# Kernel optimization log

Measured on AMD Instinct MI355X. Metric: run time of the kernel, lower is better.

The kernel has to match this reference:

```python
import jax, jax.numpy as jnp
import numpy as np

N_NODES = 100000
N_EDGES = 1600000
NUM_RELS = 16
NUM_BASES = 8
IN_FEATS = 128
N_HIDDEN = 128
N_CLASSES = 40


def _make_layer_params(key, d_in, d_out):
    k0, k1, k2 = jax.random.split(key, 3)
    s_in = 1.0 / np.sqrt(d_in)
    bases = jax.random.normal(k0, (NUM_BASES, d_in, d_out), jnp.float32) * s_in
    comp = jax.random.normal(k1, (NUM_RELS, NUM_BASES), jnp.float32) * (1.0 / np.sqrt(NUM_BASES))
    root = jax.random.normal(k2, (d_in, d_out), jnp.float32) * s_in
    bias = jnp.zeros((d_out,), jnp.float32)
    return bases, comp, root, bias


def setup_inputs() -> dict:
    key = jax.random.key(0)
    ks = jax.random.split(key, 8)
    x = jax.random.normal(ks[0], (N_NODES, IN_FEATS), jnp.float32)
    edge_src = jax.random.randint(ks[1], (N_EDGES,), 0, N_NODES, dtype=jnp.int32)
    edge_dst = jax.random.randint(ks[2], (N_EDGES,), 0, N_NODES, dtype=jnp.int32)
    edge_type = jax.random.randint(ks[3], (N_EDGES,), 0, NUM_RELS, dtype=jnp.int32)
    bases0, comp0, root0, bias0 = _make_layer_params(ks[4], IN_FEATS, N_HIDDEN)
    bases1, comp1, root1, bias1 = _make_layer_params(ks[5], N_HIDDEN, N_HIDDEN)
    bases2, comp2, root2, bias2 = _make_layer_params(ks[6], N_HIDDEN, N_CLASSES)
    return dict(x=x, edge_src=edge_src, edge_dst=edge_dst, edge_type=edge_type,
                bases0=bases0, comp0=comp0, root0=root0, bias0=bias0,
                bases1=bases1, comp1=comp1, root1=root1, bias1=bias1,
                bases2=bases2, comp2=comp2, root2=root2, bias2=bias2)


def _rgcn_layer(x, edge_src, edge_dst, edge_type, bases, comp, root, bias):
    # basis decomposition: W_r = sum_b comp[r,b] * bases[b]   -> [R, d_in, d_out]
    W = jnp.einsum('rb,bio->rio', comp, bases)
    # transform all node features under every relation (R small, dense GEMMs)
    xw = jnp.einsum('ni,rio->rno', x, W)                    # [R, N, d_out]
    # per-edge message: gather by (relation, source) -- irregular access
    msg = xw[edge_type, edge_src]                           # [E, d_out]
    # mean aggregation per (destination, relation), as in PyG RGCNConv (aggr='mean')
    seg = edge_dst * NUM_RELS + edge_type                   # [E]
    deg = jax.ops.segment_sum(jnp.ones((msg.shape[0],), x.dtype), seg,
                              num_segments=N_NODES * NUM_RELS)
    norm = 1.0 / jnp.maximum(deg[seg], 1.0)                 # [E]
    agg = jax.ops.segment_sum(msg * norm[:, None], edge_dst, num_segments=N_NODES)
    return agg + x @ root + bias


def reference(x, edge_src, edge_dst, edge_type,
              bases0, comp0, root0, bias0,
              bases1, comp1, root1, bias1,
              bases2, comp2, root2, bias2):
    # dropout is identity at inference; activation='relu' on all but last layer
    h = _rgcn_layer(x, edge_src, edge_dst, edge_type, bases0, comp0, root0, bias0)
    h = jax.nn.relu(h)
    h = _rgcn_layer(h, edge_src, edge_dst, edge_type, bases1, comp1, root1, bias1)
    h = jax.nn.relu(h)
    h = _rgcn_layer(h, edge_src, edge_dst, edge_type, bases2, comp2, root2, bias2)
    return h
```

## Files before the change

kernel.cpp:

```cpp
#include <hip/hip_runtime.h>
#include <hip/hip_bf16.h>

#define NNODES 100000
#define NEDGES 1600000
#define NRELS 16
#define NBASES 8
#define DFEAT 128
#define NCLS 40
#define MAXDEG 64
#define KTOT 1152
#define KA   1024

typedef __attribute__((ext_vector_type(8))) short bf16x8v;
typedef __attribute__((ext_vector_type(4))) float f32x4v;
typedef __attribute__((ext_vector_type(2))) float f32x2v;
typedef __attribute__((ext_vector_type(4))) unsigned short u16x4;

struct __align__(8) bf16x4s { __hip_bfloat162 lo, hi; };

__global__ __launch_bounds__(256)
void k_pre(const float* __restrict__ x, __hip_bfloat16* __restrict__ xb,
           short* __restrict__ q8, float* __restrict__ qs,
           const int* __restrict__ esrc, const int* __restrict__ edst,
           const int* __restrict__ etyp,
           unsigned* __restrict__ degD, unsigned* __restrict__ ell)
{
    unsigned bid = blockIdx.x;
    if (bid % 17u == 0u) {
        int k = (int)(bid / 17u);
        int e0 = k * 1024 + ((int)threadIdx.x << 2);
        if (e0 < NEDGES) {
            int4 s4 = *(const int4*)(esrc + e0);
            int4 d4 = *(const int4*)(edst + e0);
            int4 t4 = *(const int4*)(etyp + e0);
            unsigned sl0 = atomicAdd(&degD[d4.x], 1u);
            unsigned sl1 = atomicAdd(&degD[d4.y], 1u);
            unsigned sl2 = atomicAdd(&degD[d4.z], 1u);
            unsigned sl3 = atomicAdd(&degD[d4.w], 1u);
            if (sl0 < MAXDEG) __builtin_nontemporal_store(
                ((unsigned)s4.x << 4) | (unsigned)t4.x, &ell[(size_t)d4.x * MAXDEG + sl0]);
            if (sl1 < MAXDEG) __builtin_nontemporal_store(
                ((unsigned)s4.y << 4) | (unsigned)t4.y, &ell[(size_t)d4.y * MAXDEG + sl1]);
            if (sl2 < MAXDEG) __builtin_nontemporal_store(
                ((unsigned)s4.z << 4) | (unsigned)t4.z, &ell[(size_t)d4.z * MAXDEG + sl2]);
            if (sl3 < MAXDEG) __builtin_nontemporal_store(
                ((unsigned)s4.w << 4) | (unsigned)t4.w, &ell[(size_t)d4.w * MAXDEG + sl3]);
        }
    } else {
        int cb = (int)(bid - (bid + 16u) / 17u);
        int wave = threadIdx.x >> 6, lane = threadIdx.x & 63;
        int v = cb * 4 + wave;
        if (v >= NNODES) return;
        float2 xv = ((const float2*)x)[(size_t)v * 64 + lane];
        __hip_bfloat162 bv;
        bv.x = __float2bfloat16(xv.x);
        bv.y = __float2bfloat16(xv.y);
        ((__hip_bfloat162*)xb)[(size_t)v * 64 + lane] = bv;
        float m = fmaxf(fabsf(xv.x), fabsf(xv.y));
#pragma unroll
        for (int o = 32; o; o >>= 1) m = fmaxf(m, __shfl_xor(m, o));
        float inv = (m > 0.f) ? 127.f / m : 0.f;
        int qx = (int)rintf(xv.x * inv), qy = (int)rintf(xv.y * inv);
        q8[(size_t)v * 64 + lane] = (short)((qx & 0xff) | (qy << 8));
        if (lane == 0) qs[v] = m * (1.f / 127.f);
    }
}

__global__ __launch_bounds__(256)
void k_agg(const short* __restrict__ q8, const float* __restrict__ qs,
           const unsigned* __restrict__ ell,
           const unsigned* __restrict__ degD,
           const float* __restrict__ comp,
           __hip_bfloat16* __restrict__ A,
           int r0, int rows)
{
    __shared__ float compS[NRELS * NBASES];
    __shared__ __align__(16) float cS[8][MAXDEG][8];
    __shared__ unsigned sS[8][MAXDEG];
    __shared__ unsigned histS[8][NRELS];
    if (threadIdx.x < NRELS * NBASES) compS[threadIdx.x] = comp[threadIdx.x];
    __syncthreads();

    int wave = threadIdx.x >> 6, lane = threadIdx.x & 63;
    int half = lane >> 5, hl = lane & 31;
    int node = wave * 2 + half;
    int rl = blockIdx.x * 8 + node;
    bool alive = (rl < rows);
    int v = alive ? (r0 + rl) : 0;
    int ne = alive ? (int)degD[v] : 0; if (ne > MAXDEG) ne = MAXDEG;

    if (alive) {
        const unsigned* erow = ell + (size_t)v * MAXDEG;
        unsigned p0 = (hl < ne) ? erow[hl] : 0u;
        unsigned p1 = (hl + 32 < ne) ? erow[hl + 32] : 0u;
        if (hl < NRELS) histS[node][hl] = 0u;
        if (hl < ne)      atomicAdd(&histS[node][p0 & 15u], 1u);
        if (hl + 32 < ne) atomicAdd(&histS[node][p1 & 15u], 1u);
#pragma unroll
        for (int r = 0; r < 2; r++) {
            unsigned p = r ? p1 : p0;
            int slot = hl + 32 * r;
            bool val = (slot < ne);
            unsigned t = p & 15u;
            int s = val ? (int)(p >> 4) : 0;
            unsigned cnt = val ? histS[node][t] : 1u;
            if (cnt < 1u) cnt = 1u;
            float w = val ? (qs[s] / (float)cnt) : 0.f;
            f32x4v c0, c1;
#pragma unroll
            for (int b = 0; b < 4; b++) c0[b] = compS[t * NBASES + b] * w;
#pragma unroll
            for (int b = 0; b < 4; b++) c1[b] = compS[t * NBASES + 4 + b] * w;
            *(f32x4v*)&cS[node][slot][0] = c0;
            *(f32x4v*)&cS[node][slot][4] = c1;
            sS[node][slot] = (unsigned)s;
        }
    }

    f32x2v accA[NBASES], accB[NBASES];
#pragma unroll
    for (int b = 0; b < NBASES; b++) { accA[b] = (f32x2v){0.f,0.f}; accB[b] = (f32x2v){0.f,0.f}; }

    if (alive) {
        for (int e0 = 0; e0 < ne; e0 += 16) {
            unsigned qd[16];
#pragma unroll
            for (int j = 0; j < 16; j++) {
                unsigned s = sS[node][e0 + j];
                qd[j] = ((const unsigned*)(q8 + (size_t)s * 64))[hl];
            }
#pragma unroll
            for (int j = 0; j < 16; j++) {
                f32x4v ca = *(const f32x4v*)&cS[node][e0 + j][0];
                f32x4v cb = *(const f32x4v*)&cS[node][e0 + j][4];
                unsigned d = qd[j];
                f32x2v f01, f23;
                f01.x = (float)(char)(d & 0xff);
                f01.y = (float)(char)((d >> 8) & 0xff);
                f23.x = (float)(char)((d >> 16) & 0xff);
                f23.y = (float)(char)(d >> 24);
                accA[0] += ca[0] * f01;  accB[0] += ca[0] * f23;
                accA[1] += ca[1] * f01;  accB[1] += ca[1] * f23;
                accA[2] += ca[2] * f01;  accB[2] += ca[2] * f23;
                accA[3] += ca[3] * f01;  accB[3] += ca[3] * f23;
                accA[4] += cb[0] * f01;  accB[4] += cb[0] * f23;
                accA[5] += cb[1] * f01;  accB[5] += cb[1] * f23;
                accA[6] += cb[2] * f01;  accB[6] += cb[2] * f23;
                accA[7] += cb[3] * f01;  accB[7] += cb[3] * f23;
            }
        }
        __hip_bfloat16* Arow = A + (size_t)rl * KA;
#pragma unroll
        for (int b = 0; b < NBASES; b++) {
            bf16x4s o;
            o.lo.x = __float2bfloat16(accA[b].x);
            o.lo.y = __float2bfloat16(accA[b].y);
            o.hi.x = __float2bfloat16(accB[b].x);
            o.hi.y = __float2bfloat16(accB[b].y);
            __builtin_nontemporal_store(*(const u16x4*)&o, (u16x4*)&Arow[b * 128 + 4 * hl]);
        }
    }
}

__global__ __launch_bounds__(256)
void k_w(const float* __restrict__ bases, const float* __restrict__ root,
         __hip_bfloat16* __restrict__ WT, int dout, int npad)
{
    int idx = blockIdx.x * 256 + threadIdx.x;
    int total = npad * KTOT;
    if (idx >= total) return;
    int o = idx / KTOT, k = idx - o * KTOT;
    float v = 0.f;
    if (o < dout) v = (k < KA) ? bases[k * dout + o] : root[(k - KA) * dout + o];
    WT[idx] = __float2bfloat16(v);
}

template<int NT, bool RELU, bool FINAL>
__global__ __launch_bounds__(256)
void k_gemm(const __hip_bfloat16* __restrict__ A,
            const __hip_bfloat16* __restrict__ hroot,
            const __hip_bfloat16* __restrict__ WT,
            const float* __restrict__ bias,
            void* __restrict__ outp,
            short* __restrict__ q8o, float* __restrict__ qso,
            int r0, int rows, int dout)
{
    constexpr int WM = (NT == 128) ? 2 : 4;
    constexpr int WN = 4 / WM;
    constexpr int MT = 128 / (16 * WM);
    constexpr int NTW = NT / (16 * WN);
    __shared__ __align__(16) __hip_bfloat16 As[128 * 32];
    __shared__ __align__(16) __hip_bfloat16 Bs[NT * 32];
    __shared__ unsigned rmax[128];
    int tid = threadIdx.x;
    int wave = tid >> 6, lane = tid & 63;
    int wm = wave % WM, wn = wave / WM;
    int bm = blockIdx.x * 128;
    int lm = lane & 15, lq = lane >> 4;
    if (RELU && tid < 128) rmax[tid] = 0u;
    f32x4v zero = {0.f, 0.f, 0.f, 0.f};
    f32x4v acc[MT][NTW];
#pragma unroll
    for (int a = 0; a < MT; a++)
#pragma unroll
        for (int b = 0; b < NTW; b++) acc[a][b] = zero;

    for (int k0 = 0; k0 < KTOT; k0 += 32) {
#pragma unroll
        for (int j = 0; j < 2; j++) {
            int slot = tid + 256 * j;
            int row = slot >> 2, kc = (slot & 3) << 3;
            const __hip_bfloat16* src;
            if (k0 < KA) {
                src = &A[(size_t)(bm + row) * KA + k0 + kc];
            } else {
                int gr = r0 + bm + row; if (gr > NNODES - 1) gr = NNODES - 1;
                src = &hroot[(size_t)gr * DFEAT + (k0 - KA) + kc];
            }
            __builtin_amdgcn_global_load_lds(
                (const __attribute__((address_space(1))) void*)src,
                (__attribute__((address_space(3))) void*)&As[slot * 8],
                16, 0, 0);
        }
#pragma unroll
        for (int j = 0; j < NT / 64; j++) {
            int slot = tid + 256 * j;
            int row = slot >> 2, kc = (slot & 3) << 3;
            __builtin_amdgcn_global_load_lds(
                (const __attribute__((address_space(1))) void*)
                    &WT[(size_t)row * KTOT + k0 + kc],
                (__attribute__((address_space(3))) void*)&Bs[slot * 8],
                16, 0, 0);
        }
        __syncthreads();
        bf16x8v af[MT], bfr[NTW];
#pragma unroll
        for (int mt = 0; mt < MT; mt++)
            af[mt] = *(const bf16x8v*)&As[(wm * (16 * MT) + mt * 16 + lm) * 32 + lq * 8];
#pragma unroll
        for (int nt = 0; nt < NTW; nt++)
            bfr[nt] = *(const bf16x8v*)&Bs[(wn * (16 * NTW) + nt * 16 + lm) * 32 + lq * 8];
#pragma unroll
        for (int mt = 0; mt < MT; mt++)
#pragma unroll
            for (int nt = 0; nt < NTW; nt++)
                acc[mt][nt] = __builtin_amdgcn_mfma_f32_16x16x32_bf16(
                    af[mt], bfr[nt], acc[mt][nt], 0, 0, 0);
        __syncthreads();
    }

#pragma unroll
    for (int mt = 0; mt < MT; mt++) {
#pragma unroll
        for (int i = 0; i < 4; i++) {
            float mx = 0.f;
#pragma unroll
            for (int nt = 0; nt < NTW; nt++) {
                int col = wn * (16 * NTW) + nt * 16 + lm;
                float v = acc[mt][nt][i] + bias[col];
                if (RELU) { v = fmaxf(v, 0.f); mx = fmaxf(mx, v); }
                acc[mt][nt][i] = v;
            }
            if (RELU) {
                int lrow = wm * (16 * MT) + mt * 16 + lq * 4 + i;
                atomicMax(&rmax[lrow], __float_as_uint(mx));
            }
        }
    }
    if (RELU) __syncthreads();
#pragma unroll
    for (int mt = 0; mt < MT; mt++) {
        int rbase = bm + wm * (16 * MT) + mt * 16 + lq * 4;
#pragma unroll
        for (int i = 0; i < 4; i++) {
            int rl = rbase + i;
            if (rl >= rows) continue;
            float inv = 0.f;
            if (RELU) {
                float m = __uint_as_float(rmax[wm * (16 * MT) + mt * 16 + lq * 4 + i]);
                inv = (m > 0.f) ? 127.f / m : 0.f;
            }
#pragma unroll
            for (int nt = 0; nt < NTW; nt++) {
                int col = wn * (16 * NTW) + nt * 16 + lm;
                float v = acc[mt][nt][i];
                if (FINAL) {
                    if (col < dout)
                        ((float*)outp)[(size_t)(r0 + rl) * NCLS + col] = v;
                } else {
                    ((__hip_bfloat16*)outp)[(size_t)(r0 + rl) * DFEAT + col] =
                        __float2bfloat16(v);
                    int qv = (int)rintf(v * inv);
                    ((char*)q8o)[(size_t)(r0 + rl) * DFEAT + col] = (char)qv;
                }
            }
        }
    }
    if (RELU) {
        if (tid < 128 && bm + tid < rows)
            qso[r0 + bm + tid] = __uint_as_float(rmax[tid]) * (1.f / 127.f);
    }
}

extern "C" void kernel_launch(void* const* d_in, const int* in_sizes, int n_in,
                              void* d_out, int out_size, void* d_ws, size_t ws_size,
                              hipStream_t stream)
{
    const float* x  = (const float*)d_in[0];
    const int* esrc = (const int*)d_in[1];
    const int* edst = (const int*)d_in[2];
    const int* etyp = (const int*)d_in[3];
    const float* basesA[3] = {(const float*)d_in[4], (const float*)d_in[8], (const float*)d_in[12]};
    const float* compA[3]  = {(const float*)d_in[5], (const float*)d_in[9], (const float*)d_in[13]};
    const float* rootA[3]  = {(const float*)d_in[6], (const float*)d_in[10], (const float*)d_in[14]};
    const float* biasA[3]  = {(const float*)d_in[7], (const float*)d_in[11], (const float*)d_in[15]};

    size_t off = 0;
    char* base = (char*)d_ws;
    auto carve = [&](size_t bytes) -> void* {
        void* r = base + off;
        off += (bytes + 255) & ~(size_t)255;
        return r;
    };
    __hip_bfloat16* xb = (__hip_bfloat16*)carve((size_t)NNODES * DFEAT * 2);
    __hip_bfloat16* h1 = (__hip_bfloat16*)carve((size_t)NNODES * DFEAT * 2);
    __hip_bfloat16* WT = (__hip_bfloat16*)carve((size_t)128 * KTOT * 2);
    unsigned* ell  = (unsigned*)carve((size_t)NNODES * MAXDEG * 4);
    unsigned* degD = (unsigned*)carve((size_t)NNODES * 4);
    short* q8A = (short*)carve((size_t)NNODES * 64 * 2);
    short* q8B = (short*)carve((size_t)NNODES * 64 * 2);
    float* qsA = (float*)carve((size_t)NNODES * 4);
    float* qsB = (float*)carve((size_t)NNODES * 4);

    if (ws_size <= off) return;
    size_t arows = (ws_size - off) / ((size_t)KA * 2);
    if (arows > 100096) arows = 100096;
    int chunk = (int)(arows & ~(size_t)127);
    if (chunk < 128) return;
    __hip_bfloat16* A = (__hip_bfloat16*)(base + off);

    hipMemsetAsync(degD, 0, (size_t)NNODES * 4, stream);
    k_pre<<<26563, 256, 0, stream>>>(x, xb, q8A, qsA, esrc, edst, etyp, degD, ell);

    const __hip_bfloat16* hin = xb;
    __hip_bfloat16* houts[2] = {h1, xb};
    const short* q8in = q8A;  short* q8out = q8B;
    const float* qsin = qsA;  float* qsout = qsB;
    for (int l = 0; l < 3; l++) {
        int dout = (l == 2) ? NCLS : DFEAT;
        int npad = (l == 2) ? 64 : 128;
        k_w<<<(npad * KTOT + 255) / 256, 256, 0, stream>>>(basesA[l], rootA[l], WT, dout, npad);
        for (int r0 = 0; r0 < NNODES; r0 += chunk) {
            int rows = NNODES - r0; if (rows > chunk) rows = chunk;
            k_agg<<<(rows + 7) / 8, 256, 0, stream>>>(q8in, qsin, ell, degD, compA[l], A, r0, rows);
            int gm = (rows + 127) / 128;
            if (l < 2)
                k_gemm<128, true, false><<<gm, 256, 0, stream>>>(
                    A, hin, WT, biasA[l], houts[l], q8out, qsout, r0, rows, dout);
            else
                k_gemm<64, false, true><<<gm, 256, 0, stream>>>(
                    A, hin, WT, biasA[l], d_out, nullptr, nullptr, r0, rows, dout);
        }
        if (l < 2) {
            hin = houts[l];
            const short* tq = q8in; q8in = q8out; q8out = (short*)tq;
            const float* tf = qsin; qsin = qsout; qsout = (float*)tf;
        }
    }
}
```

Measured before the change: 741.8 us.

## Build ELL adjacency via destination bucketing and shared-memory assembly

Replaces the per-edge global atomic slot allocation and scattered ELL stores with two passes. The first pass sorts each block's edges locally into 196 destination buckets and appends packed 64-bit records to per-bucket bins. The second pass has one block per bucket assemble its 512-node ELL slab and degree counts in shared memory and write them out coalesced. This aims to cut the cost of random global atomics and scattered writes, in exchange for an extra kernel launch, more workspace, a large LDS footprint per block, and a fixed bucket capacity that would overflow on skewed graphs. It also guards the final-layer bias read against padded columns.

```diff
diff --git a/kernel.cpp b/kernel.cpp
--- a/kernel.cpp
+++ b/kernel.cpp
@@ -10,44 +10,75 @@
 #define MAXDEG 64
 #define KTOT 1152
 #define KA   1024
+#define NBUCK 196
+#define NPAD  (NBUCK * 512)
+#define BCAP  9216
 
 typedef __attribute__((ext_vector_type(8))) short bf16x8v;
 typedef __attribute__((ext_vector_type(4))) float f32x4v;
 typedef __attribute__((ext_vector_type(2))) float f32x2v;
 typedef __attribute__((ext_vector_type(4))) unsigned short u16x4;
+typedef unsigned long long u64;
 
 struct __align__(8) bf16x4s { __hip_bfloat162 lo, hi; };
 
 __global__ __launch_bounds__(256)
-void k_pre(const float* __restrict__ x, __hip_bfloat16* __restrict__ xb,
+void k_bin(const float* __restrict__ x, __hip_bfloat16* __restrict__ xb,
            short* __restrict__ q8, float* __restrict__ qs,
            const int* __restrict__ esrc, const int* __restrict__ edst,
            const int* __restrict__ etyp,
-           unsigned* __restrict__ degD, unsigned* __restrict__ ell)
+           unsigned* __restrict__ binCnt, u64* __restrict__ bins)
 {
     unsigned bid = blockIdx.x;
-    if (bid % 17u == 0u) {
-        int k = (int)(bid / 17u);
-        int e0 = k * 1024 + ((int)threadIdx.x << 2);
-        if (e0 < NEDGES) {
-            int4 s4 = *(const int4*)(esrc + e0);
-            int4 d4 = *(const int4*)(edst + e0);
-            int4 t4 = *(const int4*)(etyp + e0);
-            unsigned sl0 = atomicAdd(&degD[d4.x], 1u);
-            unsigned sl1 = atomicAdd(&degD[d4.y], 1u);
-            unsigned sl2 = atomicAdd(&degD[d4.z], 1u);
-            unsigned sl3 = atomicAdd(&degD[d4.w], 1u);
-            if (sl0 < MAXDEG) __builtin_nontemporal_store(
-                ((unsigned)s4.x << 4) | (unsigned)t4.x, &ell[(size_t)d4.x * MAXDEG + sl0]);
-            if (sl1 < MAXDEG) __builtin_nontemporal_store(
-                ((unsigned)s4.y << 4) | (unsigned)t4.y, &ell[(size_t)d4.y * MAXDEG + sl1]);
-            if (sl2 < MAXDEG) __builtin_nontemporal_store(
-                ((unsigned)s4.z << 4) | (unsigned)t4.z, &ell[(size_t)d4.z * MAXDEG + sl2]);
-            if (sl3 < MAXDEG) __builtin_nontemporal_store(
-                ((unsigned)s4.w << 4) | (unsigned)t4.w, &ell[(size_t)d4.w * MAXDEG + sl3]);
+    if (bid % 9u == 0u) {
+        __shared__ unsigned histS[NBUCK], rankS[NBUCK];
+        __shared__ unsigned baseLS[NBUCK], baseGS[NBUCK];
+        __shared__ unsigned wsumS[4];
+        __shared__ u64 recS[512];
+        int k = (int)(bid / 9u);
+        int t = threadIdx.x, lane = t & 63, wv = t >> 6;
+        for (int i = t; i < NBUCK; i += 256) { histS[i] = 0u; rankS[i] = 0u; }
+        __syncthreads();
+        int2 s2 = ((const int2*)esrc)[k * 256 + t];
+        int2 d2 = ((const int2*)edst)[k * 256 + t];
+        int2 t2 = ((const int2*)etyp)[k * 256 + t];
+        unsigned b0 = (unsigned)d2.x >> 9, b1 = (unsigned)d2.y >> 9;
+        u64 r0 = ((u64)(unsigned)d2.x << 21) | ((unsigned)s2.x << 4) | (unsigned)t2.x;
+        u64 r1 = ((u64)(unsigned)d2.y << 21) | ((unsigned)s2.y << 4) | (unsigned)t2.y;
+        atomicAdd(&histS[b0], 1u);
+        atomicAdd(&histS[b1], 1u);
+        __syncthreads();
+        unsigned h = (t < NBUCK) ? histS[t] : 0u, v = h;
+#pragma unroll
+        for (int o = 1; o < 64; o <<= 1) {
+            unsigned u = __shfl_up(v, o);
+            if (lane >= o) v += u;
+        }
+        if (lane == 63) wsumS[wv] = v;
+        __syncthreads();
+        unsigned wo = 0;
+        for (int w = 0; w < wv; w++) wo += wsumS[w];
+        v += wo;
+        if (t < NBUCK) {
+            baseLS[t] = v - h;
+            baseGS[t] = atomicAdd(&binCnt[t], h);
+        }
+        __syncthreads();
+        unsigned q0 = atomicAdd(&rankS[b0], 1u);
+        recS[baseLS[b0] + q0] = r0;
+        unsigned q1 = atomicAdd(&rankS[b1], 1u);
+        recS[baseLS[b1] + q1] = r1;
+        __syncthreads();
+#pragma unroll
+        for (int j = 0; j < 2; j++) {
+            int idx = t + 256 * j;
+            u64 rr = recS[idx];
+            unsigned bb = (unsigned)(rr >> 21) >> 9;
+            unsigned go = baseGS[bb] + ((unsigned)idx - baseLS[bb]);
+            if (go < BCAP) bins[(size_t)bb * BCAP + go] = rr;
         }
     } else {
-        int cb = (int)(bid - (bid + 16u) / 17u);
+        int cb = (int)(bid - bid / 9u - 1u);
         int wave = threadIdx.x >> 6, lane = threadIdx.x & 63;
         int v = cb * 4 + wave;
         if (v >= NNODES) return;
@@ -64,6 +95,32 @@
         q8[(size_t)v * 64 + lane] = (short)((qx & 0xff) | (qy << 8));
         if (lane == 0) qs[v] = m * (1.f / 127.f);
     }
+}
+
+__global__ __launch_bounds__(256)
+void k_ell(const u64* __restrict__ bins, const unsigned* __restrict__ binCnt,
+           unsigned* __restrict__ ell, unsigned* __restrict__ degD)
+{
+    __shared__ unsigned cntS[512];
+    __shared__ unsigned ellS[512 * MAXDEG];
+    int b = blockIdx.x, t = threadIdx.x;
+    for (int i = t; i < 512; i += 256) cntS[i] = 0u;
+    __syncthreads();
+    unsigned n = binCnt[b]; if (n > BCAP) n = BCAP;
+    const u64* rp = bins + (size_t)b * BCAP;
+    for (unsigned i = t; i < n; i += 256) {
+        u64 r = rp[i];
+        unsigned ld = ((unsigned)(r >> 21)) & 511u;
+        unsigned slot = atomicAdd(&cntS[ld], 1u);
+        if (slot < MAXDEG) ellS[ld * MAXDEG + slot] = (unsigned)(r & 0x1FFFFFu);
+    }
+    __syncthreads();
+    size_t row0 = (size_t)b << 9;
+    uint4* eo = (uint4*)(ell + row0 * MAXDEG);
+    const uint4* ei = (const uint4*)ellS;
+    for (int i = t; i < 512 * (MAXDEG / 4); i += 256)
+        eo[i] = ei[i];
+    if (t < 256) { degD[row0 + t] = cntS[t]; degD[row0 + 256 + t] = cntS[256 + t]; }
 }
 
 __global__ __launch_bounds__(256)
@@ -257,7 +314,8 @@
 #pragma unroll
             for (int nt = 0; nt < NTW; nt++) {
                 int col = wn * (16 * NTW) + nt * 16 + lm;
-                float v = acc[mt][nt][i] + bias[col];
+                float bval = (!FINAL || col < dout) ? bias[col] : 0.f;
+                float v = acc[mt][nt][i] + bval;
                 if (RELU) { v = fmaxf(v, 0.f); mx = fmaxf(mx, v); }
                 acc[mt][nt][i] = v;
             }
@@ -325,12 +383,14 @@
     __hip_bfloat16* xb = (__hip_bfloat16*)carve((size_t)NNODES * DFEAT * 2);
     __hip_bfloat16* h1 = (__hip_bfloat16*)carve((size_t)NNODES * DFEAT * 2);
     __hip_bfloat16* WT = (__hip_bfloat16*)carve((size_t)128 * KTOT * 2);
-    unsigned* ell  = (unsigned*)carve((size_t)NNODES * MAXDEG * 4);
-    unsigned* degD = (unsigned*)carve((size_t)NNODES * 4);
+    unsigned* ell  = (unsigned*)carve((size_t)NPAD * MAXDEG * 4);
+    unsigned* degD = (unsigned*)carve((size_t)NPAD * 4);
     short* q8A = (short*)carve((size_t)NNODES * 64 * 2);
     short* q8B = (short*)carve((size_t)NNODES * 64 * 2);
     float* qsA = (float*)carve((size_t)NNODES * 4);
     float* qsB = (float*)carve((size_t)NNODES * 4);
+    unsigned* binCnt = (unsigned*)carve((size_t)NBUCK * 4);
+    u64* bins = (u64*)carve((size_t)NBUCK * BCAP * 8);
 
     if (ws_size <= off) return;
     size_t arows = (ws_size - off) / ((size_t)KA * 2);
@@ -339,8 +399,9 @@
     if (chunk < 128) return;
     __hip_bfloat16* A = (__hip_bfloat16*)(base + off);
 
-    hipMemsetAsync(degD, 0, (size_t)NNODES * 4, stream);
-    k_pre<<<26563, 256, 0, stream>>>(x, xb, q8A, qsA, esrc, edst, etyp, degD, ell);
+    hipMemsetAsync(binCnt, 0, (size_t)NBUCK * 4, stream);
+    k_bin<<<28125, 256, 0, stream>>>(x, xb, q8A, qsA, esrc, edst, etyp, binCnt, bins);
+    k_ell<<<NBUCK, 256, 0, stream>>>(bins, binCnt, ell, degD);
 
     const __hip_bfloat16* hin = xb;
     __hip_bfloat16* houts[2] = {h1, xb};
```

New measurement: 719.5 us. 1.03x faster.
